# Optimization experiments

Measured on AMD Instinct MI355X. Metric: run time of the kernel, lower is better.

The kernel has to match this reference:

```python
import jax, jax.numpy as jnp
import numpy as np

H = 2048

def _lstm_layer(x, W_ih, W_hh, b_ih, b_hh):
    # x: [B,T,I]; W_ih: [4H,I]; W_hh: [4H,H]; gate order i,f,g,o (PyTorch)
    B = x.shape[0]
    x_proj = jnp.einsum('bti,gi->btg', x, W_ih) + b_ih + b_hh  # [B,T,4H]
    def step(carry, xt):
        h, c = carry
        gates = xt + h @ W_hh.T                     # [B,4H]
        i, f, g, o = jnp.split(gates, 4, axis=-1)
        i = jax.nn.sigmoid(i); f = jax.nn.sigmoid(f)
        g = jnp.tanh(g);       o = jax.nn.sigmoid(o)
        c = f * c + i * g
        h = o * jnp.tanh(c)
        return (h, c), h
    h0 = jnp.zeros((B, H), x.dtype)
    c0 = jnp.zeros((B, H), x.dtype)
    _, ys = jax.lax.scan(step, (h0, c0), x_proj.transpose(1, 0, 2))
    return ys.transpose(1, 0, 2)  # [B,T,H]

def setup_inputs() -> dict:
    key = jax.random.key(0)
    ks = jax.random.split(key, 16)
    B, T, I, O = 16, 128, 128, 1
    s = 1.0 / np.sqrt(H)
    def u(k, shape):
        return jax.random.uniform(k, shape, jnp.float32, -s, s)
    inp = {"x": jax.random.normal(ks[0], (B, T, I), jnp.float32)}
    in_dims = [I, H, H]
    for l in range(3):
        inp[f"W_ih{l}"] = u(ks[1 + 4 * l], (4 * H, in_dims[l]))
        inp[f"W_hh{l}"] = u(ks[2 + 4 * l], (4 * H, H))
        inp[f"b_ih{l}"] = u(ks[3 + 4 * l], (4 * H,))
        inp[f"b_hh{l}"] = u(ks[4 + 4 * l], (4 * H,))
    inp["W_out"] = u(ks[13], (O, H))
    inp["b_out"] = u(ks[14], (O,))
    return inp

def reference(x, W_ih0, W_hh0, b_ih0, b_hh0,
              W_ih1, W_hh1, b_ih1, b_hh1,
              W_ih2, W_hh2, b_ih2, b_hh2,
              W_out, b_out):
    h = _lstm_layer(x, W_ih0, W_hh0, b_ih0, b_hh0)
    h = _lstm_layer(h, W_ih1, W_hh1, b_ih1, b_hh1)
    h = _lstm_layer(h, W_ih2, W_hh2, b_ih2, b_hh2)
    return h @ W_out.T + b_out  # [B,T,O]
```

## Files before the change

### kernel.cpp

```cpp
#include <hip/hip_runtime.h>
#include <hip/hip_fp16.h>
#include <cstdint>
#include <cstddef>


typedef __attribute__((ext_vector_type(8))) _Float16 fp16x8;
typedef __attribute__((ext_vector_type(4))) float    f32x4;

#define HDIM  2048
#define GATES 8192
#define BATCH 16
#define TSEQ  128
#define NTOK  2048
#define RED_ST 17
#define HSLOT 128
#define HSTEP_ELEMS 32768
#define FLAG_STRIDE 16
#define NFLAG_COPY 4
#define FB_OFF (NFLAG_COPY * 256 * FLAG_STRIDE)
#define W_LDS_BYTES 131072

union HU { _Float16 f; unsigned short u; };

__device__ __forceinline__ float sigmoidf_(float x) { return 1.f / (1.f + __expf(-x)); }
__device__ __forceinline__ float tanhf_(float x) {
    float e2 = __expf(2.f * x);
    return 1.f - 2.f / (e2 + 1.f);
}

__global__ __launch_bounds__(256) void cvt_f32_f16_kernel(const float* __restrict__ in,
                                                          _Float16* __restrict__ out, int n8) {
    int i = blockIdx.x * 256 + threadIdx.x;
    if (i >= n8) return;
    const float4* p = (const float4*)in + (size_t)i * 2;
    float4 a = p[0], b = p[1];
    fp16x8 v;
    v[0] = (_Float16)a.x; v[1] = (_Float16)a.y; v[2] = (_Float16)a.z; v[3] = (_Float16)a.w;
    v[4] = (_Float16)b.x; v[5] = (_Float16)b.y; v[6] = (_Float16)b.z; v[7] = (_Float16)b.w;
    ((fp16x8*)out)[i] = v;
}

__global__ __launch_bounds__(256) void xproj_gemm_kernel(
        const _Float16* __restrict__ A, const _Float16* __restrict__ Ah,
        const _Float16* __restrict__ W,
        const float* __restrict__ bih, const float* __restrict__ bhh,
        float* __restrict__ xp, int K) {
    __shared__ _Float16 As[128 * 64];
    __shared__ _Float16 Bs[128 * 64];
    const int tid  = threadIdx.x;
    const int lane = tid & 63;
    const int wave = tid >> 6;
    const int n0 = blockIdx.x * 128;
    const int m0 = blockIdx.y * 128;
    const int srow = tid >> 3;
    const int scol = (tid & 7) * 8;
    const int wr = (wave >> 1) * 64;
    const int wc = (wave & 1) * 64;
    const int lr = lane & 15;
    const int lk = (lane >> 4) * 8;

    f32x4 acc[4][4] = {};

    const int nk = K >> 6;
    for (int kt = 0; kt < nk; ++kt) {
        if (kt) __syncthreads();
        const int k0 = kt * 64;
#pragma unroll
        for (int cc = 0; cc < 4; ++cc) {
            const int row = cc * 32 + srow;
            const _Float16* ga;
            if (Ah) {
                const int m = m0 + row, b = m >> 7, tt = m & 127;
                ga = Ah + (size_t)(tt + 1) * HSTEP_ELEMS + (size_t)(k0 + scol) * 16 + b * 8;
            } else {
                ga = A + (size_t)(m0 + row) * K + k0 + scol;
            }
            const _Float16* gb = W + (size_t)(n0 + row) * K + k0 + scol;
            __builtin_amdgcn_global_load_lds(
                (const __attribute__((address_space(1))) void*)ga,
                (__attribute__((address_space(3))) void*)(As + cc * 2048 + wave * 512), 16, 0, 0);
            __builtin_amdgcn_global_load_lds(
                (const __attribute__((address_space(1))) void*)gb,
                (__attribute__((address_space(3))) void*)(Bs + cc * 2048 + wave * 512), 16, 0, 0);
        }
        __syncthreads();
#pragma unroll
        for (int s = 0; s < 2; ++s) {
            fp16x8 af[4], bf[4];
#pragma unroll
            for (int mi = 0; mi < 4; ++mi)
                af[mi] = *(const fp16x8*)(As + (wr + mi * 16 + lr) * 64 + s * 32 + lk);
#pragma unroll
            for (int ni = 0; ni < 4; ++ni)
                bf[ni] = *(const fp16x8*)(Bs + (wc + ni * 16 + lr) * 64 + s * 32 + lk);
#pragma unroll
            for (int mi = 0; mi < 4; ++mi)
#pragma unroll
                for (int ni = 0; ni < 4; ++ni)
                    acc[mi][ni] = __builtin_amdgcn_mfma_f32_16x16x32_f16(
                        af[mi], bf[ni], acc[mi][ni], 0, 0, 0);
        }
    }
    const int rb = (lane >> 4) * 4;
#pragma unroll
    for (int ni = 0; ni < 4; ++ni) {
        const int n = n0 + wc + ni * 16 + lr;
        const float bias = bih[n] + bhh[n];
#pragma unroll
        for (int mi = 0; mi < 4; ++mi) {
#pragma unroll
            for (int r = 0; r < 4; ++r) {
                const int m = m0 + wr + mi * 16 + rb + r;
                const int b = m >> 7, t = m & 127;
                xp[((size_t)t * BATCH + b) * GATES + n] = acc[mi][ni][r] + bias;
            }
        }
    }
}

__global__ __launch_bounds__(256, 1) void lstm_scan_kernel(
        const float* __restrict__ Whh,
        const float* __restrict__ xp,
        _Float16* __restrict__ hstep,
        int* __restrict__ flags,
        int flag_base) {
    __builtin_amdgcn_fence(__ATOMIC_ACQUIRE, "agent");

    extern __shared__ char smemW[];
    __shared__ float red[2][8 * 16 * RED_ST];

    const int tid  = threadIdx.x;
    const int lane = tid & 63;
    const int wave = tid >> 6;
    const int blk  = blockIdx.x;
    const int h0   = blk * 8;
    const int ln15 = lane & 15;
    const int kl   = (lane >> 4) * 8;
    const int kbase = wave * 512;

    for (int r = 0; r < 32; ++r) {
        const float* wrow = Whh + ((size_t)((r >> 3) * HDIM + h0 + (r & 7))) * HDIM;
        const int c = tid * 8;
        float4 f0 = *(const float4*)(wrow + c);
        float4 f1 = *(const float4*)(wrow + c + 4);
        fp16x8 v;
        v[0] = (_Float16)f0.x; v[1] = (_Float16)f0.y; v[2] = (_Float16)f0.z; v[3] = (_Float16)f0.w;
        v[4] = (_Float16)f1.x; v[5] = (_Float16)f1.y; v[6] = (_Float16)f1.z; v[7] = (_Float16)f1.w;
        uint32_t byte = ((uint32_t)(r * 4096 + c * 2)) ^ ((uint32_t)((r & 7) << 4));
        *(fp16x8*)(smemW + byte) = v;
    }

    float c_state = 0.f;
    const int uh = tid & 7, ub = tid >> 3;

    const uint32_t sw     = (uint32_t)((ln15 & 7) << 4);
    const uint32_t r0base = (uint32_t)ln15 * 4096u;
    const uint32_t r1base = r0base + 16u * 4096u;

    const int pidx = ((blk & 3) << 8) | (wave << 6) | lane;
    const int* fa = flags + (size_t)pidx * FLAG_STRIDE;
    const int* fb = fa + FB_OFF;

    __syncthreads();

    for (int t = 0; t < TSEQ; ++t) {
        if (t) {
            while (__hip_atomic_load(fa, __ATOMIC_RELAXED, __HIP_MEMORY_SCOPE_AGENT) < flag_base + t ||
                   __hip_atomic_load(fb, __ATOMIC_RELAXED, __HIP_MEMORY_SCOPE_AGENT) < flag_base + t) {}
        }
        asm volatile("" ::: "memory");
        const _Float16* hsrc = hstep + (size_t)t * HSTEP_ELEMS;

        fp16x8 af[16];
#pragma unroll
        for (int s = 0; s < 16; ++s) {
            const int k = kbase + s * 32 + kl;
            af[s] = *(const fp16x8*)(hsrc + (size_t)k * 16 + ln15 * 8);
        }
        float xi = 0.f, xf = 0.f, xg = 0.f, xo = 0.f;
        if (tid < 128) {
            const float* xpt = xp + ((size_t)t * BATCH + ub) * GATES + h0 + uh;
            xi = xpt[0];
            xf = xpt[HDIM];
            xg = xpt[2 * HDIM];
            xo = xpt[3 * HDIM];
        }

        f32x4 a0e = {0.f,0.f,0.f,0.f}, a0o = {0.f,0.f,0.f,0.f};
        f32x4 a1e = {0.f,0.f,0.f,0.f}, a1o = {0.f,0.f,0.f,0.f};
#pragma unroll
        for (int s = 0; s < 16; s += 2) {
            const uint32_t kb  = (uint32_t)((kbase + s * 32 + kl) * 2);
            const uint32_t kb1 = kb + 64;
            fp16x8 w0e = *(const fp16x8*)(smemW + ((r0base + kb ) ^ sw));
            fp16x8 w1e = *(const fp16x8*)(smemW + ((r1base + kb ) ^ sw));
            fp16x8 w0o = *(const fp16x8*)(smemW + ((r0base + kb1) ^ sw));
            fp16x8 w1o = *(const fp16x8*)(smemW + ((r1base + kb1) ^ sw));
            a0e = __builtin_amdgcn_mfma_f32_16x16x32_f16(af[s],     w0e, a0e, 0, 0, 0);
            a1e = __builtin_amdgcn_mfma_f32_16x16x32_f16(af[s],     w1e, a1e, 0, 0, 0);
            a0o = __builtin_amdgcn_mfma_f32_16x16x32_f16(af[s + 1], w0o, a0o, 0, 0, 0);
            a1o = __builtin_amdgcn_mfma_f32_16x16x32_f16(af[s + 1], w1o, a1o, 0, 0, 0);
        }
        f32x4 acc0 = a0e + a0o;
        f32x4 acc1 = a1e + a1o;
        {
            float* r0 = red[t & 1] + ((wave * 2 + 0) * 16 + ln15) * RED_ST + (lane >> 4) * 4;
            float* r1 = red[t & 1] + ((wave * 2 + 1) * 16 + ln15) * RED_ST + (lane >> 4) * 4;
#pragma unroll
            for (int i = 0; i < 4; ++i) { r0[i] = acc0[i]; r1[i] = acc1[i]; }
        }
        __syncthreads();
        asm volatile("" ::: "memory");

        if (tid < 128) {
            const float* redp = red[t & 1];
            float ip = xi, fp_ = xf, gp = xg, op = xo;
#pragma unroll
            for (int w = 0; w < 4; ++w) {
                ip  += redp[((w * 2 + 0) * 16 + uh    ) * RED_ST + ub];
                fp_ += redp[((w * 2 + 0) * 16 + uh + 8) * RED_ST + ub];
                gp  += redp[((w * 2 + 1) * 16 + uh    ) * RED_ST + ub];
                op  += redp[((w * 2 + 1) * 16 + uh + 8) * RED_ST + ub];
            }
            float ig = sigmoidf_(ip), fg = sigmoidf_(fp_), og = sigmoidf_(op);
            float gg = tanhf_(gp);
            c_state = fg * c_state + ig * gg;
            float hv = og * tanhf_(c_state);
            HU cv; cv.f = (_Float16)hv;
            unsigned v  = cv.u;
            unsigned v1 = __shfl_down(v, 1, 64);
            unsigned v2 = __shfl_down(v, 2, 64);
            unsigned v3 = __shfl_down(v, 3, 64);
            if ((tid & 3) == 0) {
                unsigned long long pk = (unsigned long long)v
                                      | ((unsigned long long)v1 << 16)
                                      | ((unsigned long long)v2 << 32)
                                      | ((unsigned long long)v3 << 48);
                unsigned long long* dst = (unsigned long long*)
                    (hstep + (size_t)(t + 1) * HSTEP_ELEMS + blk * HSLOT + ub * 8 + uh);
                __hip_atomic_store(dst, pk, __ATOMIC_RELAXED, __HIP_MEMORY_SCOPE_AGENT);
            }
            if (t < TSEQ - 1) {
                asm volatile("s_waitcnt vmcnt(0)" ::: "memory");
                if (lane == 0) {
                    int* base = flags + (wave ? FB_OFF : 0);
#pragma unroll
                    for (int c = 0; c < NFLAG_COPY; ++c)
                        __hip_atomic_store(base + (size_t)((c << 8) | blk) * FLAG_STRIDE,
                                           flag_base + t + 1,
                                           __ATOMIC_RELAXED, __HIP_MEMORY_SCOPE_AGENT);
                }
            }
        }
    }
}

__global__ __launch_bounds__(256) void outproj_kernel(
        const _Float16* __restrict__ hstep, const float* __restrict__ Wout,
        const float* __restrict__ bout, float* __restrict__ out) {
    const int lane = threadIdx.x & 63;
    const int wave = threadIdx.x >> 6;
    const int tok = blockIdx.x * 4 + wave;
    const int b = tok >> 7, t = tok & 127;
    const _Float16* h = hstep + (size_t)(t + 1) * HSTEP_ELEMS + b * 8;
    float acc = 0.f;
#pragma unroll
    for (int c = 0; c < 4; ++c) {
        const int k = c * 512 + lane * 8;
        fp16x8 hv = *(const fp16x8*)(h + (size_t)k * 16);
        const float* w = Wout + k;
#pragma unroll
        for (int i = 0; i < 8; ++i) acc += (float)hv[i] * w[i];
    }
#pragma unroll
    for (int off = 32; off > 0; off >>= 1) acc += __shfl_down(acc, off, 64);
    if (lane == 0) out[tok] = acc + bout[0];
}

extern "C" void kernel_launch(void* const* d_in, const int* in_sizes, int n_in,
                              void* d_out, int out_size, void* d_ws, size_t ws_size,
                              hipStream_t stream) {
    (void)in_sizes; (void)n_in; (void)out_size; (void)ws_size;
    const float* x       = (const float*)d_in[0];
    const float* Wih[3]  = {(const float*)d_in[1], (const float*)d_in[5], (const float*)d_in[9]};
    const float* Whh[3]  = {(const float*)d_in[2], (const float*)d_in[6], (const float*)d_in[10]};
    const float* bih[3]  = {(const float*)d_in[3], (const float*)d_in[7], (const float*)d_in[11]};
    const float* bhh[3]  = {(const float*)d_in[4], (const float*)d_in[8], (const float*)d_in[12]};
    const float* Wout    = (const float*)d_in[13];
    const float* bout    = (const float*)d_in[14];
    float* out = (float*)d_out;

    char* ws = (char*)d_ws;
    size_t off = 0;
    auto carve = [&](size_t bytes) {
        char* p = ws + off;
        off += (bytes + 255) & ~(size_t)255;
        return p;
    };
    _Float16* wih16 = (_Float16*)carve((size_t)GATES * 2048 * 2);
    float*    xp    = (float*)   carve((size_t)TSEQ * GATES * BATCH * 4);
    _Float16* xh    = (_Float16*)carve((size_t)NTOK * 128 * 2);
    _Float16* hstep = (_Float16*)carve((size_t)(TSEQ + 1) * HSTEP_ELEMS * 2);
    int*      flags = (int*)     carve((size_t)2 * NFLAG_COPY * 256 * FLAG_STRIDE * 4);

    hipFuncSetAttribute((const void*)lstm_scan_kernel,
                        hipFuncAttributeMaxDynamicSharedMemorySize, W_LDS_BYTES);

    hipMemsetAsync(flags, 0, (size_t)2 * NFLAG_COPY * 256 * FLAG_STRIDE * 4, stream);
    hipMemsetAsync(hstep, 0, HSTEP_ELEMS * 2, stream);

    {
        int n8 = NTOK * 128 / 8;
        cvt_f32_f16_kernel<<<(n8 + 255) / 256, 256, 0, stream>>>(x, xh, n8);
    }

    const int Kl[3] = {128, 2048, 2048};
    for (int l = 0; l < 3; ++l) {
        int n8 = GATES * Kl[l] / 8;
        cvt_f32_f16_kernel<<<(n8 + 255) / 256, 256, 0, stream>>>(Wih[l], wih16, n8);
        dim3 ggrid(GATES / 128, NTOK / 128);
        xproj_gemm_kernel<<<ggrid, 256, 0, stream>>>(
            l == 0 ? xh : nullptr, l == 0 ? nullptr : hstep,
            wih16, bih[l], bhh[l], xp, Kl[l]);
        lstm_scan_kernel<<<256, 256, W_LDS_BYTES, stream>>>(Whh[l], xp, hstep, flags, l * TSEQ);
    }
    outproj_kernel<<<NTOK / 4, 256, 0, stream>>>(hstep, Wout, bout, out);
}
```

Measured before the change: 1.827 ms.

## Fuse next-layer W_ih fp16 conversion into the recurrent scan kernel

Removes the standalone weight conversion launches for layers 1 and 2. The scan kernel instead converts slices of the next layer's W_ih to fp16 during its first 32 timesteps. The conversion loads are issued before the flag spin-wait so they overlap with idle synchronization time. This adds memory traffic to the latency-critical recurrent loop, which could slow the per-step critical path. The spin loop is also lightly restructured.

```diff
diff --git a/kernel.cpp b/kernel.cpp
--- a/kernel.cpp
+++ b/kernel.cpp
@@ -123,7 +123,9 @@
         const float* __restrict__ xp,
         _Float16* __restrict__ hstep,
         int* __restrict__ flags,
-        int flag_base) {
+        int flag_base,
+        const float* __restrict__ Wih_nx,
+        _Float16* __restrict__ wih_out) {
     __builtin_amdgcn_fence(__ATOMIC_ACQUIRE, "agent");
 
     extern __shared__ char smemW[];
@@ -161,12 +163,26 @@
     const int* fa = flags + (size_t)pidx * FLAG_STRIDE;
     const int* fb = fa + FB_OFF;
 
+    const size_t cvt_base = ((size_t)blk * 256 + tid) * 32;
+
     __syncthreads();
 
     for (int t = 0; t < TSEQ; ++t) {
+        const bool docvt = (Wih_nx != nullptr) && (t < 32);
+        float4 cw0, cw1;
+        if (docvt) {
+            const float* src = Wih_nx + (cvt_base + t) * 8;
+            cw0 = *(const float4*)src;
+            cw1 = *(const float4*)(src + 4);
+        }
+
         if (t) {
-            while (__hip_atomic_load(fa, __ATOMIC_RELAXED, __HIP_MEMORY_SCOPE_AGENT) < flag_base + t ||
-                   __hip_atomic_load(fb, __ATOMIC_RELAXED, __HIP_MEMORY_SCOPE_AGENT) < flag_base + t) {}
+            const int want = flag_base + t;
+            int va, vb;
+            do {
+                va = __hip_atomic_load(fa, __ATOMIC_RELAXED, __HIP_MEMORY_SCOPE_AGENT);
+                vb = __hip_atomic_load(fb, __ATOMIC_RELAXED, __HIP_MEMORY_SCOPE_AGENT);
+            } while (va < want || vb < want);
         }
         asm volatile("" ::: "memory");
         const _Float16* hsrc = hstep + (size_t)t * HSTEP_ELEMS;
@@ -252,6 +268,14 @@
                 }
             }
         }
+        if (docvt) {
+            fp16x8 v;
+            v[0] = (_Float16)cw0.x; v[1] = (_Float16)cw0.y;
+            v[2] = (_Float16)cw0.z; v[3] = (_Float16)cw0.w;
+            v[4] = (_Float16)cw1.x; v[5] = (_Float16)cw1.y;
+            v[6] = (_Float16)cw1.z; v[7] = (_Float16)cw1.w;
+            *(fp16x8*)(wih_out + (cvt_base + t) * 8) = v;
+        }
     }
 }
 
@@ -313,16 +337,20 @@
         int n8 = NTOK * 128 / 8;
         cvt_f32_f16_kernel<<<(n8 + 255) / 256, 256, 0, stream>>>(x, xh, n8);
     }
+    {
+        int n8 = GATES * 128 / 8;
+        cvt_f32_f16_kernel<<<(n8 + 255) / 256, 256, 0, stream>>>(Wih[0], wih16, n8);
+    }
 
     const int Kl[3] = {128, 2048, 2048};
     for (int l = 0; l < 3; ++l) {
-        int n8 = GATES * Kl[l] / 8;
-        cvt_f32_f16_kernel<<<(n8 + 255) / 256, 256, 0, stream>>>(Wih[l], wih16, n8);
         dim3 ggrid(GATES / 128, NTOK / 128);
         xproj_gemm_kernel<<<ggrid, 256, 0, stream>>>(
             l == 0 ? xh : nullptr, l == 0 ? nullptr : hstep,
             wih16, bih[l], bhh[l], xp, Kl[l]);
-        lstm_scan_kernel<<<256, 256, W_LDS_BYTES, stream>>>(Whh[l], xp, hstep, flags, l * TSEQ);
+        lstm_scan_kernel<<<256, 256, W_LDS_BYTES, stream>>>(
+            Whh[l], xp, hstep, flags, l * TSEQ,
+            l < 2 ? Wih[l + 1] : nullptr, wih16);
     }
     outproj_kernel<<<NTOK / 4, 256, 0, stream>>>(hstep, Wout, bout, out);
 }
```

After: 1.808 ms. About the same (-1.1%).
